# Optimization experiments

Measured on AMD Instinct MI355X. Metric: run time of the kernel, lower is better.

The kernel has to match this reference:

```python
import jax, jax.numpy as jnp
import numpy as np

N = 262144  # nodes
E = 262144  # edges (child -> parent)
X = 128     # x_size
H = 128     # h_size


def setup_inputs() -> dict:
    key = jax.random.key(0)
    ks = jax.random.split(key, 10)
    s = 1.0 / np.sqrt(H)
    return {
        "token_embeds": jax.random.normal(ks[0], (N, X), jnp.float32),
        "h": jax.random.normal(ks[1], (N, H), jnp.float32),
        "c": jax.random.normal(ks[2], (N, H), jnp.float32),
        "src": jax.random.randint(ks[3], (E,), 0, N),
        "dst": jax.random.randint(ks[4], (E,), 0, N),
        "W_iou": jax.random.normal(ks[5], (3 * H, X), jnp.float32) * s,
        "U_iou": jax.random.normal(ks[6], (3 * H, H), jnp.float32) * s,
        "b_iou": jnp.zeros((1, 3 * H), jnp.float32),
        "U_f_w": jax.random.normal(ks[7], (H, H), jnp.float32) * s,
        "U_f_b": jnp.zeros((H,), jnp.float32),
        "W_f_w": jax.random.normal(ks[8], (H, X), jnp.float32) * s,
        "b_f": jnp.zeros((1, H), jnp.float32),
    }


def reference(token_embeds, h, c, src, dst, W_iou, U_iou, b_iou, U_f_w, U_f_b, W_f_w, b_f):
    # message + reduce: gather children's h/c and sum into parent mailboxes
    h_sum = jax.ops.segment_sum(h[src], dst, num_segments=N)  # [N,H]
    c_sum = jax.ops.segment_sum(c[src], dst, num_segments=N)  # [N,H]
    # forget gate is per-node, so sum_k f*c_k == f * sum_k c_k
    f = jax.nn.sigmoid(token_embeds @ W_f_w.T + h @ U_f_w.T + U_f_b + b_f)  # [N,H]
    c_red = f * c_sum
    iou = token_embeds @ W_iou.T + h_sum @ U_iou.T + b_iou  # [N,3H]
    i, o, u = jnp.split(iou, 3, axis=1)
    c_new = jax.nn.sigmoid(i) * jnp.tanh(u) + c_red
    h_new = jax.nn.sigmoid(o) * jnp.tanh(c_new)
    return h_new, c_new
```

## Files before the change

kernel.cpp:

```cpp
#include <hip/hip_runtime.h>
#include <hip/hip_bf16.h>
#include <cstdint>

#define HH 128
#define XX 128

typedef __attribute__((ext_vector_type(8))) short short8;
typedef __attribute__((ext_vector_type(4))) short short4_;
typedef __attribute__((ext_vector_type(4))) float float4_;
typedef __attribute__((ext_vector_type(8))) _Float16 half8_;

__device__ __forceinline__ float sigmoidf_(float x) {
  return 1.f / (1.f + __expf(-x));
}
__device__ __forceinline__ float tanhf_(float x) {
  float e = __expf(-2.f * fabsf(x));
  float t = (1.f - e) / (1.f + e);
  return copysignf(t, x);
}

__global__ __launch_bounds__(256) void hist_kernel(const int* __restrict__ dst,
                                                   int* __restrict__ cnt, int E) {
  int e = blockIdx.x * 256 + threadIdx.x;
  if (e < E) atomicAdd(&cnt[dst[e]], 1);
}

__global__ __launch_bounds__(256) void scan_block_sum(const int* __restrict__ cnt,
                                                      int* __restrict__ bsum) {
  __shared__ int red[256];
  int b = blockIdx.x, t = threadIdx.x;
  int base = b * 1024 + t * 4;
  int s = cnt[base] + cnt[base + 1] + cnt[base + 2] + cnt[base + 3];
  red[t] = s;
  __syncthreads();
  for (int off = 128; off > 0; off >>= 1) {
    if (t < off) red[t] += red[t + off];
    __syncthreads();
  }
  if (t == 0) bsum[b] = red[0];
}

__global__ __launch_bounds__(256) void scan_top(const int* __restrict__ bsum,
                                                int* __restrict__ boff,
                                                int* __restrict__ row_ptr, int N,
                                                int E) {
  __shared__ int tmp[256];
  int t = threadIdx.x;
  int own = bsum[t];
  tmp[t] = own;
  __syncthreads();
  for (int off = 1; off < 256; off <<= 1) {
    int x = (t >= off) ? tmp[t - off] : 0;
    __syncthreads();
    tmp[t] += x;
    __syncthreads();
  }
  boff[t] = tmp[t] - own;
  if (t == 0) row_ptr[N] = E;
}

__global__ __launch_bounds__(256) void scan_fill(const int* __restrict__ cnt,
                                                 const int* __restrict__ boff,
                                                 int* __restrict__ row_ptr,
                                                 int* __restrict__ row_fill) {
  __shared__ int tsum[256];
  int b = blockIdx.x, t = threadIdx.x;
  int base = b * 1024 + t * 4;
  int v0 = cnt[base], v1 = cnt[base + 1], v2 = cnt[base + 2], v3 = cnt[base + 3];
  int s = v0 + v1 + v2 + v3;
  tsum[t] = s;
  __syncthreads();
  for (int off = 1; off < 256; off <<= 1) {
    int x = (t >= off) ? tsum[t - off] : 0;
    __syncthreads();
    tsum[t] += x;
    __syncthreads();
  }
  int excl = tsum[t] - s + boff[b];
  int p0 = excl, p1 = p0 + v0, p2 = p1 + v1, p3 = p2 + v2;
  row_ptr[base] = p0;
  row_ptr[base + 1] = p1;
  row_ptr[base + 2] = p2;
  row_ptr[base + 3] = p3;
  row_fill[base] = p0;
  row_fill[base + 1] = p1;
  row_fill[base + 2] = p2;
  row_fill[base + 3] = p3;
}

__global__ __launch_bounds__(256) void fill_kernel(const int* __restrict__ src,
                                                   const int* __restrict__ dst,
                                                   int* __restrict__ row_fill,
                                                   int* __restrict__ edge_src,
                                                   int E) {
  int e = blockIdx.x * 256 + threadIdx.x;
  if (e >= E) return;
  int pos = atomicAdd(&row_fill[dst[e]], 1);
  edge_src[pos] = src[e];
}

__global__ __launch_bounds__(256) void prep_kernel(
    const float* __restrict__ W_iou, const float* __restrict__ U_iou,
    const float* __restrict__ b_iou, const float* __restrict__ U_f_w,
    const float* __restrict__ U_f_b, const float* __restrict__ W_f_w,
    const float* __restrict__ b_f, unsigned short* __restrict__ Bh,
    float* __restrict__ bias) {
  int tid = blockIdx.x * 256 + threadIdx.x;
  int kg = tid & 3;
  int c16 = (tid >> 2) & 15;
  int ks = (tid >> 6) & 7;
  int w = (tid >> 9) & 7;
  int g = (tid >> 12) & 3;
  int col = w * 16 + c16;
  int kbase = ks * 32 + kg * 8;
#pragma unroll
  for (int j = 0; j < 8; ++j) {
    int k = kbase + j;
    float v;
    if (g < 3) {
      v = (k < 128) ? W_iou[(size_t)(g * 128 + col) * 128 + k]
                    : U_iou[(size_t)(g * 128 + col) * 128 + (k - 128)];
    } else {
      v = (k < 128) ? W_f_w[(size_t)col * 128 + k]
                    : U_f_w[(size_t)col * 128 + (k - 128)];
    }
    Bh[(size_t)tid * 8 + j] = __builtin_bit_cast(unsigned short, (_Float16)v);
  }
  if (tid < 512) {
    int gg = tid >> 7, cc = tid & 127;
    bias[tid] = (gg < 3) ? b_iou[gg * 128 + cc] : (U_f_b[cc] + b_f[cc]);
  }
}


__device__ __forceinline__ void stage_f16(unsigned short* su, int a, int node,
                                          int k4, float4_ v) {
  unsigned short hq[4];
#pragma unroll
  for (int j = 0; j < 4; ++j)
    hq[j] = __builtin_bit_cast(unsigned short, (_Float16)v[j]);
  int off = k4 ^ ((node & 7) << 3);
  *reinterpret_cast<short4_*>(&su[a * 8192 + node * 128 + off]) =
      *reinterpret_cast<const short4_*>(hq);
}

__device__ __forceinline__ half8_ read_frag(const unsigned short* su, int a,
                                            int node, int kbase, int lane) {
  int k = kbase + ((lane >> 4) << 3);
  int off = k ^ ((node & 7) << 3);
  short8 s = *reinterpret_cast<const short8*>(&su[a * 8192 + node * 128 + off]);
  return __builtin_bit_cast(half8_, s);
}

__device__ __forceinline__ int cw(int row, int col) {
  return row * 128 + (col ^ ((row & 7) << 2));
}

__global__ __launch_bounds__(512, 4) void fused_mfma_kernel(
    const float* __restrict__ te, const float* __restrict__ h,
    const float* __restrict__ c, const int* __restrict__ row_ptr,
    const int* __restrict__ edge_src, const unsigned short* __restrict__ Bh,
    const float* __restrict__ bias, float* __restrict__ out_h,
    float* __restrict__ out_c) {
  __shared__ float4_ smem4[5120];
  unsigned short* su = (unsigned short*)smem4;
  float* cf = (float*)smem4 + 12288;

  const int t = threadIdx.x;
  const int node0 = blockIdx.x * 64;

  const int nl = t >> 3;
  const int sub = t & 7;
  const int e0 = row_ptr[node0 + nl];
  const int e1 = row_ptr[node0 + nl + 1];
  int s0 = (e0 < e1) ? edge_src[e0] : 0;
  float4_ ph[4], pc[4];
  if (e0 < e1) {
    const float* hp = h + (size_t)s0 * HH + sub * 16;
    const float* cp = c + (size_t)s0 * HH + sub * 16;
#pragma unroll
    for (int i = 0; i < 4; ++i) {
      ph[i] = *reinterpret_cast<const float4_*>(hp + i * 4);
      pc[i] = *reinterpret_cast<const float4_*>(cp + i * 4);
    }
  }

#pragma unroll
  for (int i = 0; i < 4; ++i) {
    int q = t + i * 512;
    int node = q >> 5;
    int k4 = (q & 31) * 4;
    float4_ v =
        *reinterpret_cast<const float4_*>(te + (size_t)(node0 + node) * XX + k4);
    stage_f16(su, 0, node, k4, v);
    v = *reinterpret_cast<const float4_*>(h + (size_t)(node0 + node) * HH + k4);
    stage_f16(su, 2, node, k4, v);
  }

  {
    float hs[16], cs[16];
#pragma unroll
    for (int j = 0; j < 16; ++j) {
      hs[j] = 0.f;
      cs[j] = 0.f;
    }
    if (e0 < e1) {
#pragma unroll
      for (int i = 0; i < 4; ++i)
#pragma unroll
        for (int j = 0; j < 4; ++j) {
          hs[i * 4 + j] += ph[i][j];
          cs[i * 4 + j] += pc[i][j];
        }
    }
    for (int e = e0 + 1; e < e1; ++e) {
      int s = edge_src[e];
      const float* hp = h + (size_t)s * HH + sub * 16;
      const float* cp = c + (size_t)s * HH + sub * 16;
#pragma unroll
      for (int i = 0; i < 4; ++i) {
        float4_ hv = *reinterpret_cast<const float4_*>(hp + i * 4);
        float4_ cv = *reinterpret_cast<const float4_*>(cp + i * 4);
#pragma unroll
        for (int j = 0; j < 4; ++j) {
          hs[i * 4 + j] += hv[j];
          cs[i * 4 + j] += cv[j];
        }
      }
    }
#pragma unroll
    for (int i = 0; i < 4; ++i) {
      float4_ v = {hs[i * 4], hs[i * 4 + 1], hs[i * 4 + 2], hs[i * 4 + 3]};
      stage_f16(su, 1, nl, sub * 16 + i * 4, v);
      *reinterpret_cast<float4_*>(&cf[cw(nl, sub * 16 + i * 4)]) =
          (float4_){cs[i * 4], cs[i * 4 + 1], cs[i * 4 + 2], cs[i * 4 + 3]};
    }
  }
  __syncthreads();

  const int lane = t & 63;
  const int wave = t >> 6;
  const int wc = wave * 16;
  const int cl = lane & 15;
  const int kq = lane >> 4;

  float4_ acc[4][4];
#pragma unroll
  for (int g = 0; g < 4; ++g) {
    float b = bias[g * 128 + wc + cl];
#pragma unroll
    for (int m = 0; m < 4; ++m) acc[g][m] = (float4_){b, b, b, b};
  }

  for (int ks = 0; ks < 8; ++ks) {
    half8_ bh[4];
#pragma unroll
    for (int g = 0; g < 4; ++g) {
      size_t boff = (size_t)(((g * 8 + wave) * 8 + ks) * 512) + cl * 32 + kq * 8;
      bh[g] = __builtin_bit_cast(half8_,
                                 *reinterpret_cast<const short8*>(&Bh[boff]));
    }
    if (ks < 4) {
      int kbase = ks * 32;
#pragma unroll
      for (int m = 0; m < 4; ++m) {
        half8_ ah = read_frag(su, 0, m * 16 + cl, kbase, lane);
#pragma unroll
        for (int g = 0; g < 4; ++g)
          acc[g][m] =
              __builtin_amdgcn_mfma_f32_16x16x32_f16(ah, bh[g], acc[g][m], 0, 0, 0);
      }
    } else {
      int kbase = (ks - 4) * 32;
#pragma unroll
      for (int m = 0; m < 4; ++m) {
        half8_ ah = read_frag(su, 1, m * 16 + cl, kbase, lane);
        half8_ fh = read_frag(su, 2, m * 16 + cl, kbase, lane);
#pragma unroll
        for (int g = 0; g < 3; ++g)
          acc[g][m] =
              __builtin_amdgcn_mfma_f32_16x16x32_f16(ah, bh[g], acc[g][m], 0, 0, 0);
        acc[3][m] =
            __builtin_amdgcn_mfma_f32_16x16x32_f16(fh, bh[3], acc[3][m], 0, 0, 0);
      }
    }
  }

  float csv[4][4];
#pragma unroll
  for (int m = 0; m < 4; ++m)
#pragma unroll
    for (int r = 0; r < 4; ++r)
      csv[m][r] = cf[cw(m * 16 + kq * 4 + r, wc + cl)];

  __syncthreads();

  float* oh = (float*)smem4;
  float* oc = (float*)smem4 + 8192;

#pragma unroll
  for (int m = 0; m < 4; ++m) {
#pragma unroll
    for (int r = 0; r < 4; ++r) {
      int rowl = m * 16 + kq * 4 + r;
      float ig = sigmoidf_(acc[0][m][r]);
      float og = sigmoidf_(acc[1][m][r]);
      float ug = tanhf_(acc[2][m][r]);
      float fg = sigmoidf_(acc[3][m][r]);
      float cn = fmaf(ig, ug, fg * csv[m][r]);
      int wadr = cw(rowl, wc + cl);
      oc[wadr] = cn;
      oh[wadr] = og * tanhf_(cn);
    }
  }
  __syncthreads();

#pragma unroll
  for (int i = 0; i < 4; ++i) {
    int q = t + i * 512;
    int rr = q >> 5;
    int k4 = (q & 31) * 4;
    int wadr = rr * 128 + (k4 ^ ((rr & 7) << 2));
    *reinterpret_cast<float4_*>(out_h + (size_t)(node0 + rr) * HH + k4) =
        *reinterpret_cast<const float4_*>(&oh[wadr]);
    *reinterpret_cast<float4_*>(out_c + (size_t)(node0 + rr) * HH + k4) =
        *reinterpret_cast<const float4_*>(&oc[wadr]);
  }
}

extern "C" void kernel_launch(void* const* d_in, const int* in_sizes, int n_in,
                              void* d_out, int out_size, void* d_ws, size_t ws_size,
                              hipStream_t stream) {
  const float* te = (const float*)d_in[0];
  const float* h = (const float*)d_in[1];
  const float* c = (const float*)d_in[2];
  const int* src = (const int*)d_in[3];
  const int* dst = (const int*)d_in[4];
  const float* W_iou = (const float*)d_in[5];
  const float* U_iou = (const float*)d_in[6];
  const float* b_iou = (const float*)d_in[7];
  const float* U_f_w = (const float*)d_in[8];
  const float* U_f_b = (const float*)d_in[9];
  const float* W_f_w = (const float*)d_in[10];
  const float* b_f = (const float*)d_in[11];

  const int N = in_sizes[1] / HH;
  const int E = in_sizes[3];

  float* out_h = (float*)d_out;
  float* out_c = out_h + (size_t)N * HH;

  char* ws = (char*)d_ws;
  unsigned short* Bh = (unsigned short*)ws;
  float* bias = (float*)(Bh + 4 * 8 * 8 * 16 * 4 * 8);
  int* cnt = (int*)(bias + 512);
  int* row_ptr = cnt + N;
  int* row_fill = row_ptr + N + 4;
  int* edge_src = row_fill + N;
  int* bsum = edge_src + E;
  int* boff = bsum + 256;

  hipMemsetAsync(cnt, 0, (size_t)N * sizeof(int), stream);

  hist_kernel<<<(E + 255) / 256, 256, 0, stream>>>(dst, cnt, E);
  scan_block_sum<<<N / 1024, 256, 0, stream>>>(cnt, bsum);
  scan_top<<<1, 256, 0, stream>>>(bsum, boff, row_ptr, N, E);
  scan_fill<<<N / 1024, 256, 0, stream>>>(cnt, boff, row_ptr, row_fill);
  fill_kernel<<<(E + 255) / 256, 256, 0, stream>>>(src, dst, row_fill, edge_src, E);

  prep_kernel<<<64, 256, 0, stream>>>(W_iou, U_iou, b_iou, U_f_w, U_f_b, W_f_w,
                                      b_f, Bh, bias);

  fused_mfma_kernel<<<N / 64, 512, 0, stream>>>(te, h, c, row_ptr, edge_src, Bh,
                                                bias, out_h, out_c);
}
```

Baseline: 289.5 us.

## Halve node tile per block and stage child c-sum in fp16 LDS

```diff
diff --git a/kernel.cpp b/kernel.cpp
--- a/kernel.cpp
+++ b/kernel.cpp
@@ -140,7 +140,7 @@
   for (int j = 0; j < 4; ++j)
     hq[j] = __builtin_bit_cast(unsigned short, (_Float16)v[j]);
   int off = k4 ^ ((node & 7) << 3);
-  *reinterpret_cast<short4_*>(&su[a * 8192 + node * 128 + off]) =
+  *reinterpret_cast<short4_*>(&su[a * 4096 + node * 128 + off]) =
       *reinterpret_cast<const short4_*>(hq);
 }
 
@@ -148,7 +148,7 @@
                                             int node, int kbase, int lane) {
   int k = kbase + ((lane >> 4) << 3);
   int off = k ^ ((node & 7) << 3);
-  short8 s = *reinterpret_cast<const short8*>(&su[a * 8192 + node * 128 + off]);
+  short8 s = *reinterpret_cast<const short8*>(&su[a * 4096 + node * 128 + off]);
   return __builtin_bit_cast(half8_, s);
 }
 
@@ -156,18 +156,17 @@
   return row * 128 + (col ^ ((row & 7) << 2));
 }
 
-__global__ __launch_bounds__(512, 4) void fused_mfma_kernel(
+__global__ __launch_bounds__(256, 5) void fused_mfma_kernel(
     const float* __restrict__ te, const float* __restrict__ h,
     const float* __restrict__ c, const int* __restrict__ row_ptr,
     const int* __restrict__ edge_src, const unsigned short* __restrict__ Bh,
     const float* __restrict__ bias, float* __restrict__ out_h,
     float* __restrict__ out_c) {
-  __shared__ float4_ smem4[5120];
+  __shared__ float4_ smem4[2048];
   unsigned short* su = (unsigned short*)smem4;
-  float* cf = (float*)smem4 + 12288;
 
   const int t = threadIdx.x;
-  const int node0 = blockIdx.x * 64;
+  const int node0 = blockIdx.x * 32;
 
   const int nl = t >> 3;
   const int sub = t & 7;
@@ -187,7 +186,7 @@
 
 #pragma unroll
   for (int i = 0; i < 4; ++i) {
-    int q = t + i * 512;
+    int q = t + i * 256;
     int node = q >> 5;
     int k4 = (q & 31) * 4;
     float4_ v =
@@ -232,92 +231,110 @@
     for (int i = 0; i < 4; ++i) {
       float4_ v = {hs[i * 4], hs[i * 4 + 1], hs[i * 4 + 2], hs[i * 4 + 3]};
       stage_f16(su, 1, nl, sub * 16 + i * 4, v);
-      *reinterpret_cast<float4_*>(&cf[cw(nl, sub * 16 + i * 4)]) =
-          (float4_){cs[i * 4], cs[i * 4 + 1], cs[i * 4 + 2], cs[i * 4 + 3]};
+      float4_ cv = {cs[i * 4], cs[i * 4 + 1], cs[i * 4 + 2], cs[i * 4 + 3]};
+      stage_f16(su, 3, nl, sub * 16 + i * 4, cv);
     }
   }
   __syncthreads();
 
   const int lane = t & 63;
   const int wave = t >> 6;
-  const int wc = wave * 16;
+  const int wc = wave * 32;
   const int cl = lane & 15;
   const int kq = lane >> 4;
 
-  float4_ acc[4][4];
-#pragma unroll
-  for (int g = 0; g < 4; ++g) {
-    float b = bias[g * 128 + wc + cl];
-#pragma unroll
-    for (int m = 0; m < 4; ++m) acc[g][m] = (float4_){b, b, b, b};
-  }
+  float4_ acc[4][2][2];
+#pragma unroll
+  for (int g = 0; g < 4; ++g)
+#pragma unroll
+    for (int cg = 0; cg < 2; ++cg) {
+      float b = bias[g * 128 + wc + cg * 16 + cl];
+      acc[g][0][cg] = (float4_){b, b, b, b};
+      acc[g][1][cg] = (float4_){b, b, b, b};
+    }
 
   for (int ks = 0; ks < 8; ++ks) {
-    half8_ bh[4];
-#pragma unroll
-    for (int g = 0; g < 4; ++g) {
-      size_t boff = (size_t)(((g * 8 + wave) * 8 + ks) * 512) + cl * 32 + kq * 8;
-      bh[g] = __builtin_bit_cast(half8_,
-                                 *reinterpret_cast<const short8*>(&Bh[boff]));
-    }
+    half8_ bh[4][2];
+#pragma unroll
+    for (int g = 0; g < 4; ++g)
+#pragma unroll
+      for (int cg = 0; cg < 2; ++cg) {
+        size_t boff =
+            (size_t)(((g * 8 + wave * 2 + cg) * 8 + ks) * 512) + cl * 32 + kq * 8;
+        bh[g][cg] = __builtin_bit_cast(
+            half8_, *reinterpret_cast<const short8*>(&Bh[boff]));
+      }
     if (ks < 4) {
       int kbase = ks * 32;
 #pragma unroll
-      for (int m = 0; m < 4; ++m) {
+      for (int m = 0; m < 2; ++m) {
         half8_ ah = read_frag(su, 0, m * 16 + cl, kbase, lane);
 #pragma unroll
         for (int g = 0; g < 4; ++g)
-          acc[g][m] =
-              __builtin_amdgcn_mfma_f32_16x16x32_f16(ah, bh[g], acc[g][m], 0, 0, 0);
+#pragma unroll
+          for (int cg = 0; cg < 2; ++cg)
+            acc[g][m][cg] = __builtin_amdgcn_mfma_f32_16x16x32_f16(
+                ah, bh[g][cg], acc[g][m][cg], 0, 0, 0);
       }
     } else {
       int kbase = (ks - 4) * 32;
 #pragma unroll
-      for (int m = 0; m < 4; ++m) {
+      for (int m = 0; m < 2; ++m) {
         half8_ ah = read_frag(su, 1, m * 16 + cl, kbase, lane);
         half8_ fh = read_frag(su, 2, m * 16 + cl, kbase, lane);
 #pragma unroll
-        for (int g = 0; g < 3; ++g)
-          acc[g][m] =
-              __builtin_amdgcn_mfma_f32_16x16x32_f16(ah, bh[g], acc[g][m], 0, 0, 0);
-        acc[3][m] =
-            __builtin_amdgcn_mfma_f32_16x16x32_f16(fh, bh[3], acc[3][m], 0, 0, 0);
-      }
-    }
-  }
-
-  float csv[4][4];
-#pragma unroll
-  for (int m = 0; m < 4; ++m)
-#pragma unroll
-    for (int r = 0; r < 4; ++r)
-      csv[m][r] = cf[cw(m * 16 + kq * 4 + r, wc + cl)];
+        for (int cg = 0; cg < 2; ++cg) {
+#pragma unroll
+          for (int g = 0; g < 3; ++g)
+            acc[g][m][cg] = __builtin_amdgcn_mfma_f32_16x16x32_f16(
+                ah, bh[g][cg], acc[g][m][cg], 0, 0, 0);
+          acc[3][m][cg] = __builtin_amdgcn_mfma_f32_16x16x32_f16(
+              fh, bh[3][cg], acc[3][m][cg], 0, 0, 0);
+        }
+      }
+    }
+  }
+
+  float csv[2][2][4];
+#pragma unroll
+  for (int m = 0; m < 2; ++m)
+#pragma unroll
+    for (int cg = 0; cg < 2; ++cg)
+#pragma unroll
+      for (int r = 0; r < 4; ++r) {
+        int row = m * 16 + kq * 4 + r;
+        int col = wc + cg * 16 + cl;
+        unsigned short hb = su[3 * 4096 + row * 128 + (col ^ ((row & 7) << 3))];
+        csv[m][cg][r] = (float)__builtin_bit_cast(_Float16, hb);
+      }
 
   __syncthreads();
 
   float* oh = (float*)smem4;
-  float* oc = (float*)smem4 + 8192;
-
-#pragma unroll
-  for (int m = 0; m < 4; ++m) {
-#pragma unroll
-    for (int r = 0; r < 4; ++r) {
-      int rowl = m * 16 + kq * 4 + r;
-      float ig = sigmoidf_(acc[0][m][r]);
-      float og = sigmoidf_(acc[1][m][r]);
-      float ug = tanhf_(acc[2][m][r]);
-      float fg = sigmoidf_(acc[3][m][r]);
-      float cn = fmaf(ig, ug, fg * csv[m][r]);
-      int wadr = cw(rowl, wc + cl);
-      oc[wadr] = cn;
-      oh[wadr] = og * tanhf_(cn);
-    }
-  }
+  float* oc = (float*)smem4 + 4096;
+
+#pragma unroll
+  for (int m = 0; m < 2; ++m)
+#pragma unroll
+    for (int cg = 0; cg < 2; ++cg)
+#pragma unroll
+      for (int r = 0; r < 4; ++r) {
+        int rowl = m * 16 + kq * 4 + r;
+        int col = wc + cg * 16 + cl;
+        float ig = sigmoidf_(acc[0][m][cg][r]);
+        float og = sigmoidf_(acc[1][m][cg][r]);
+        float ug = tanhf_(acc[2][m][cg][r]);
+        float fg = sigmoidf_(acc[3][m][cg][r]);
+        float cn = fmaf(ig, ug, fg * csv[m][cg][r]);
+        int wadr = cw(rowl, col);
+        oc[wadr] = cn;
+        oh[wadr] = og * tanhf_(cn);
+      }
   __syncthreads();
 
 #pragma unroll
   for (int i = 0; i < 4; ++i) {
-    int q = t + i * 512;
+    int q = t + i * 256;
     int rr = q >> 5;
     int k4 = (q & 31) * 4;
     int wadr = rr * 128 + (k4 ^ ((rr & 7) << 2));
@@ -371,6 +388,6 @@
   prep_kernel<<<64, 256, 0, stream>>>(W_iou, U_iou, b_iou, U_f_w, U_f_b, W_f_w,
                                       b_f, Bh, bias);
 
-  fused_mfma_kernel<<<N / 64, 512, 0, stream>>>(te, h, c, row_ptr, edge_src, Bh,
+  fused_mfma_kernel<<<N / 32, 256, 0, stream>>>(te, h, c, row_ptr, edge_src, Bh,
                                                 bias, out_h, out_c);
 }
```

Result: slower. 673.3 us (+132.5%).

## Halve node tile to 32 and store c-sum as fp16 to raise occupancy

Applied to the files above, without the earlier changes.

```diff
diff --git a/kernel.cpp b/kernel.cpp
--- a/kernel.cpp
+++ b/kernel.cpp
@@ -140,7 +140,7 @@
   for (int j = 0; j < 4; ++j)
     hq[j] = __builtin_bit_cast(unsigned short, (_Float16)v[j]);
   int off = k4 ^ ((node & 7) << 3);
-  *reinterpret_cast<short4_*>(&su[a * 8192 + node * 128 + off]) =
+  *reinterpret_cast<short4_*>(&su[a * 4096 + node * 128 + off]) =
       *reinterpret_cast<const short4_*>(hq);
 }
 
@@ -148,7 +148,7 @@
                                             int node, int kbase, int lane) {
   int k = kbase + ((lane >> 4) << 3);
   int off = k ^ ((node & 7) << 3);
-  short8 s = *reinterpret_cast<const short8*>(&su[a * 8192 + node * 128 + off]);
+  short8 s = *reinterpret_cast<const short8*>(&su[a * 4096 + node * 128 + off]);
   return __builtin_bit_cast(half8_, s);
 }
 
@@ -156,37 +156,36 @@
   return row * 128 + (col ^ ((row & 7) << 2));
 }
 
-__global__ __launch_bounds__(512, 4) void fused_mfma_kernel(
+__global__ __launch_bounds__(512, 6) void fused_mfma_kernel(
     const float* __restrict__ te, const float* __restrict__ h,
     const float* __restrict__ c, const int* __restrict__ row_ptr,
     const int* __restrict__ edge_src, const unsigned short* __restrict__ Bh,
     const float* __restrict__ bias, float* __restrict__ out_h,
     float* __restrict__ out_c) {
-  __shared__ float4_ smem4[5120];
+  __shared__ float4_ smem4[2048];
   unsigned short* su = (unsigned short*)smem4;
-  float* cf = (float*)smem4 + 12288;
 
   const int t = threadIdx.x;
-  const int node0 = blockIdx.x * 64;
-
-  const int nl = t >> 3;
-  const int sub = t & 7;
+  const int node0 = blockIdx.x * 32;
+
+  const int nl = t >> 4;
+  const int sub = t & 15;
   const int e0 = row_ptr[node0 + nl];
   const int e1 = row_ptr[node0 + nl + 1];
   int s0 = (e0 < e1) ? edge_src[e0] : 0;
-  float4_ ph[4], pc[4];
+  float4_ ph[2], pc[2];
   if (e0 < e1) {
-    const float* hp = h + (size_t)s0 * HH + sub * 16;
-    const float* cp = c + (size_t)s0 * HH + sub * 16;
-#pragma unroll
-    for (int i = 0; i < 4; ++i) {
+    const float* hp = h + (size_t)s0 * HH + sub * 8;
+    const float* cp = c + (size_t)s0 * HH + sub * 8;
+#pragma unroll
+    for (int i = 0; i < 2; ++i) {
       ph[i] = *reinterpret_cast<const float4_*>(hp + i * 4);
       pc[i] = *reinterpret_cast<const float4_*>(cp + i * 4);
     }
   }
 
 #pragma unroll
-  for (int i = 0; i < 4; ++i) {
+  for (int i = 0; i < 2; ++i) {
     int q = t + i * 512;
     int node = q >> 5;
     int k4 = (q & 31) * 4;
@@ -198,15 +197,15 @@
   }
 
   {
-    float hs[16], cs[16];
-#pragma unroll
-    for (int j = 0; j < 16; ++j) {
+    float hs[8], cs[8];
+#pragma unroll
+    for (int j = 0; j < 8; ++j) {
       hs[j] = 0.f;
       cs[j] = 0.f;
     }
     if (e0 < e1) {
 #pragma unroll
-      for (int i = 0; i < 4; ++i)
+      for (int i = 0; i < 2; ++i)
 #pragma unroll
         for (int j = 0; j < 4; ++j) {
           hs[i * 4 + j] += ph[i][j];
@@ -215,10 +214,10 @@
     }
     for (int e = e0 + 1; e < e1; ++e) {
       int s = edge_src[e];
-      const float* hp = h + (size_t)s * HH + sub * 16;
-      const float* cp = c + (size_t)s * HH + sub * 16;
-#pragma unroll
-      for (int i = 0; i < 4; ++i) {
+      const float* hp = h + (size_t)s * HH + sub * 8;
+      const float* cp = c + (size_t)s * HH + sub * 8;
+#pragma unroll
+      for (int i = 0; i < 2; ++i) {
         float4_ hv = *reinterpret_cast<const float4_*>(hp + i * 4);
         float4_ cv = *reinterpret_cast<const float4_*>(cp + i * 4);
 #pragma unroll
@@ -229,11 +228,11 @@
       }
     }
 #pragma unroll
-    for (int i = 0; i < 4; ++i) {
+    for (int i = 0; i < 2; ++i) {
       float4_ v = {hs[i * 4], hs[i * 4 + 1], hs[i * 4 + 2], hs[i * 4 + 3]};
-      stage_f16(su, 1, nl, sub * 16 + i * 4, v);
-      *reinterpret_cast<float4_*>(&cf[cw(nl, sub * 16 + i * 4)]) =
-          (float4_){cs[i * 4], cs[i * 4 + 1], cs[i * 4 + 2], cs[i * 4 + 3]};
+      stage_f16(su, 1, nl, sub * 8 + i * 4, v);
+      float4_ cv = {cs[i * 4], cs[i * 4 + 1], cs[i * 4 + 2], cs[i * 4 + 3]};
+      stage_f16(su, 3, nl, sub * 8 + i * 4, cv);
     }
   }
   __syncthreads();
@@ -244,13 +243,11 @@
   const int cl = lane & 15;
   const int kq = lane >> 4;
 
-  float4_ acc[4][4];
-#pragma unroll
-  for (int g = 0; g < 4; ++g) {
-    float b = bias[g * 128 + wc + cl];
-#pragma unroll
-    for (int m = 0; m < 4; ++m) acc[g][m] = (float4_){b, b, b, b};
-  }
+  float4_ acc[4][2];
+#pragma unroll
+  for (int g = 0; g < 4; ++g)
+#pragma unroll
+    for (int m = 0; m < 2; ++m) acc[g][m] = (float4_){0.f, 0.f, 0.f, 0.f};
 
   for (int ks = 0; ks < 8; ++ks) {
     half8_ bh[4];
@@ -263,60 +260,67 @@
     if (ks < 4) {
       int kbase = ks * 32;
 #pragma unroll
-      for (int m = 0; m < 4; ++m) {
+      for (int m = 0; m < 2; ++m) {
         half8_ ah = read_frag(su, 0, m * 16 + cl, kbase, lane);
 #pragma unroll
         for (int g = 0; g < 4; ++g)
-          acc[g][m] =
-              __builtin_amdgcn_mfma_f32_16x16x32_f16(ah, bh[g], acc[g][m], 0, 0, 0);
+          acc[g][m] = __builtin_amdgcn_mfma_f32_16x16x32_f16(ah, bh[g],
+                                                             acc[g][m], 0, 0, 0);
       }
     } else {
       int kbase = (ks - 4) * 32;
 #pragma unroll
-      for (int m = 0; m < 4; ++m) {
+      for (int m = 0; m < 2; ++m) {
         half8_ ah = read_frag(su, 1, m * 16 + cl, kbase, lane);
         half8_ fh = read_frag(su, 2, m * 16 + cl, kbase, lane);
 #pragma unroll
         for (int g = 0; g < 3; ++g)
-          acc[g][m] =
-              __builtin_amdgcn_mfma_f32_16x16x32_f16(ah, bh[g], acc[g][m], 0, 0, 0);
-        acc[3][m] =
-            __builtin_amdgcn_mfma_f32_16x16x32_f16(fh, bh[3], acc[3][m], 0, 0, 0);
+          acc[g][m] = __builtin_amdgcn_mfma_f32_16x16x32_f16(ah, bh[g],
+                                                             acc[g][m], 0, 0, 0);
+        acc[3][m] = __builtin_amdgcn_mfma_f32_16x16x32_f16(fh, bh[3],
+                                                           acc[3][m], 0, 0, 0);
       }
     }
   }
 
-  float csv[4][4];
-#pragma unroll
-  for (int m = 0; m < 4; ++m)
-#pragma unroll
-    for (int r = 0; r < 4; ++r)
-      csv[m][r] = cf[cw(m * 16 + kq * 4 + r, wc + cl)];
+  const int col = wc + cl;
+  float bi = bias[0 * 128 + col];
+  float bo = bias[1 * 128 + col];
+  float bu = bias[2 * 128 + col];
+  float bf = bias[3 * 128 + col];
+  float csv[2][4];
+#pragma unroll
+  for (int m = 0; m < 2; ++m)
+#pragma unroll
+    for (int r = 0; r < 4; ++r) {
+      int row = m * 16 + kq * 4 + r;
+      unsigned short hb = su[3 * 4096 + row * 128 + (col ^ ((row & 7) << 3))];
+      csv[m][r] = (float)__builtin_bit_cast(_Float16, hb);
+    }
 
   __syncthreads();
 
   float* oh = (float*)smem4;
-  float* oc = (float*)smem4 + 8192;
-
-#pragma unroll
-  for (int m = 0; m < 4; ++m) {
+  float* oc = (float*)smem4 + 4096;
+
+#pragma unroll
+  for (int m = 0; m < 2; ++m)
 #pragma unroll
     for (int r = 0; r < 4; ++r) {
       int rowl = m * 16 + kq * 4 + r;
-      float ig = sigmoidf_(acc[0][m][r]);
-      float og = sigmoidf_(acc[1][m][r]);
-      float ug = tanhf_(acc[2][m][r]);
-      float fg = sigmoidf_(acc[3][m][r]);
+      float ig = sigmoidf_(acc[0][m][r] + bi);
+      float og = sigmoidf_(acc[1][m][r] + bo);
+      float ug = tanhf_(acc[2][m][r] + bu);
+      float fg = sigmoidf_(acc[3][m][r] + bf);
       float cn = fmaf(ig, ug, fg * csv[m][r]);
-      int wadr = cw(rowl, wc + cl);
+      int wadr = cw(rowl, col);
       oc[wadr] = cn;
       oh[wadr] = og * tanhf_(cn);
     }
-  }
-  __syncthreads();
-
-#pragma unroll
-  for (int i = 0; i < 4; ++i) {
+  __syncthreads();
+
+#pragma unroll
+  for (int i = 0; i < 2; ++i) {
     int q = t + i * 512;
     int rr = q >> 5;
     int k4 = (q & 31) * 4;
@@ -371,6 +375,6 @@
   prep_kernel<<<64, 256, 0, stream>>>(W_iou, U_iou, b_iou, U_f_w, U_f_b, W_f_w,
                                       b_f, Bh, bias);
 
-  fused_mfma_kernel<<<N / 64, 512, 0, stream>>>(te, h, c, row_ptr, edge_src, Bh,
+  fused_mfma_kernel<<<N / 32, 512, 0, stream>>>(te, h, c, row_ptr, edge_src, Bh,
                                                 bias, out_h, out_c);
 }
```

Result: slower. 321.9 us (+11.2%).

## Load MFMA A-fragments for te and h directly from global, shrink LDS to fp16

Applied to the files above, without the earlier changes.

```diff
diff --git a/kernel.cpp b/kernel.cpp
--- a/kernel.cpp
+++ b/kernel.cpp
@@ -6,9 +6,9 @@
 #define XX 128
 
 typedef __attribute__((ext_vector_type(8))) short short8;
-typedef __attribute__((ext_vector_type(4))) short short4_;
 typedef __attribute__((ext_vector_type(4))) float float4_;
 typedef __attribute__((ext_vector_type(8))) _Float16 half8_;
+typedef __attribute__((ext_vector_type(4))) unsigned int uint4_;
 
 __device__ __forceinline__ float sigmoidf_(float x) {
   return 1.f / (1.f + __expf(-x));
@@ -133,27 +133,30 @@
 }
 
 
-__device__ __forceinline__ void stage_f16(unsigned short* su, int a, int node,
-                                          int k4, float4_ v) {
-  unsigned short hq[4];
-#pragma unroll
-  for (int j = 0; j < 4; ++j)
-    hq[j] = __builtin_bit_cast(unsigned short, (_Float16)v[j]);
-  int off = k4 ^ ((node & 7) << 3);
-  *reinterpret_cast<short4_*>(&su[a * 8192 + node * 128 + off]) =
-      *reinterpret_cast<const short4_*>(hq);
-}
-
-__device__ __forceinline__ half8_ read_frag(const unsigned short* su, int a,
+__device__ __forceinline__ uint4_ pack8(const float* v) {
+  uint4_ r;
+#pragma unroll
+  for (int i = 0; i < 4; ++i)
+    r[i] = __builtin_bit_cast(unsigned int,
+                              __builtin_amdgcn_cvt_pkrtz(v[2 * i], v[2 * i + 1]));
+  return r;
+}
+
+__device__ __forceinline__ half8_ cvt8(float4_ a, float4_ b) {
+  uint4_ u;
+  u[0] = __builtin_bit_cast(unsigned int, __builtin_amdgcn_cvt_pkrtz(a[0], a[1]));
+  u[1] = __builtin_bit_cast(unsigned int, __builtin_amdgcn_cvt_pkrtz(a[2], a[3]));
+  u[2] = __builtin_bit_cast(unsigned int, __builtin_amdgcn_cvt_pkrtz(b[0], b[1]));
+  u[3] = __builtin_bit_cast(unsigned int, __builtin_amdgcn_cvt_pkrtz(b[2], b[3]));
+  return __builtin_bit_cast(half8_, u);
+}
+
+__device__ __forceinline__ half8_ read_frag(const unsigned short* su, int baseH,
                                             int node, int kbase, int lane) {
   int k = kbase + ((lane >> 4) << 3);
   int off = k ^ ((node & 7) << 3);
-  short8 s = *reinterpret_cast<const short8*>(&su[a * 8192 + node * 128 + off]);
+  short8 s = *reinterpret_cast<const short8*>(&su[baseH + node * 128 + off]);
   return __builtin_bit_cast(half8_, s);
-}
-
-__device__ __forceinline__ int cw(int row, int col) {
-  return row * 128 + (col ^ ((row & 7) << 2));
 }
 
 __global__ __launch_bounds__(512, 4) void fused_mfma_kernel(
@@ -162,58 +165,24 @@
     const int* __restrict__ edge_src, const unsigned short* __restrict__ Bh,
     const float* __restrict__ bias, float* __restrict__ out_h,
     float* __restrict__ out_c) {
-  __shared__ float4_ smem4[5120];
+  __shared__ float4_ smem4[2048];
   unsigned short* su = (unsigned short*)smem4;
-  float* cf = (float*)smem4 + 12288;
 
   const int t = threadIdx.x;
   const int node0 = blockIdx.x * 64;
 
-  const int nl = t >> 3;
-  const int sub = t & 7;
-  const int e0 = row_ptr[node0 + nl];
-  const int e1 = row_ptr[node0 + nl + 1];
-  int s0 = (e0 < e1) ? edge_src[e0] : 0;
-  float4_ ph[4], pc[4];
-  if (e0 < e1) {
-    const float* hp = h + (size_t)s0 * HH + sub * 16;
-    const float* cp = c + (size_t)s0 * HH + sub * 16;
-#pragma unroll
-    for (int i = 0; i < 4; ++i) {
-      ph[i] = *reinterpret_cast<const float4_*>(hp + i * 4);
-      pc[i] = *reinterpret_cast<const float4_*>(cp + i * 4);
-    }
-  }
-
-#pragma unroll
-  for (int i = 0; i < 4; ++i) {
-    int q = t + i * 512;
-    int node = q >> 5;
-    int k4 = (q & 31) * 4;
-    float4_ v =
-        *reinterpret_cast<const float4_*>(te + (size_t)(node0 + node) * XX + k4);
-    stage_f16(su, 0, node, k4, v);
-    v = *reinterpret_cast<const float4_*>(h + (size_t)(node0 + node) * HH + k4);
-    stage_f16(su, 2, node, k4, v);
-  }
-
   {
+    const int nl = t >> 3;
+    const int sub = t & 7;
+    const int e0 = row_ptr[node0 + nl];
+    const int e1 = row_ptr[node0 + nl + 1];
     float hs[16], cs[16];
 #pragma unroll
     for (int j = 0; j < 16; ++j) {
       hs[j] = 0.f;
       cs[j] = 0.f;
     }
-    if (e0 < e1) {
-#pragma unroll
-      for (int i = 0; i < 4; ++i)
-#pragma unroll
-        for (int j = 0; j < 4; ++j) {
-          hs[i * 4 + j] += ph[i][j];
-          cs[i * 4 + j] += pc[i][j];
-        }
-    }
-    for (int e = e0 + 1; e < e1; ++e) {
+    for (int e = e0; e < e1; ++e) {
       int s = edge_src[e];
       const float* hp = h + (size_t)s * HH + sub * 16;
       const float* cp = c + (size_t)s * HH + sub * 16;
@@ -229,11 +198,10 @@
       }
     }
 #pragma unroll
-    for (int i = 0; i < 4; ++i) {
-      float4_ v = {hs[i * 4], hs[i * 4 + 1], hs[i * 4 + 2], hs[i * 4 + 3]};
-      stage_f16(su, 1, nl, sub * 16 + i * 4, v);
-      *reinterpret_cast<float4_*>(&cf[cw(nl, sub * 16 + i * 4)]) =
-          (float4_){cs[i * 4], cs[i * 4 + 1], cs[i * 4 + 2], cs[i * 4 + 3]};
+    for (int i = 0; i < 2; ++i) {
+      int off = (sub * 16 + i * 8) ^ ((nl & 7) << 3);
+      *reinterpret_cast<uint4_*>(&su[nl * 128 + off]) = pack8(hs + i * 8);
+      *reinterpret_cast<uint4_*>(&su[8192 + nl * 128 + off]) = pack8(cs + i * 8);
     }
   }
   __syncthreads();
@@ -243,14 +211,16 @@
   const int wc = wave * 16;
   const int cl = lane & 15;
   const int kq = lane >> 4;
+  const int col = wc + cl;
+
+  const float* teF = te + (size_t)(node0 + cl) * XX + kq * 8;
+  const float* hF = h + (size_t)(node0 + cl) * HH + kq * 8;
 
   float4_ acc[4][4];
 #pragma unroll
-  for (int g = 0; g < 4; ++g) {
-    float b = bias[g * 128 + wc + cl];
-#pragma unroll
-    for (int m = 0; m < 4; ++m) acc[g][m] = (float4_){b, b, b, b};
-  }
+  for (int g = 0; g < 4; ++g)
+#pragma unroll
+    for (int m = 0; m < 4; ++m) acc[g][m] = (float4_){0.f, 0.f, 0.f, 0.f};
 
   for (int ks = 0; ks < 8; ++ks) {
     half8_ bh[4];
@@ -264,67 +234,83 @@
       int kbase = ks * 32;
 #pragma unroll
       for (int m = 0; m < 4; ++m) {
-        half8_ ah = read_frag(su, 0, m * 16 + cl, kbase, lane);
+        const float* p = teF + (size_t)m * 16 * XX + kbase;
+        half8_ ah = cvt8(*reinterpret_cast<const float4_*>(p),
+                         *reinterpret_cast<const float4_*>(p + 4));
 #pragma unroll
         for (int g = 0; g < 4; ++g)
-          acc[g][m] =
-              __builtin_amdgcn_mfma_f32_16x16x32_f16(ah, bh[g], acc[g][m], 0, 0, 0);
+          acc[g][m] = __builtin_amdgcn_mfma_f32_16x16x32_f16(ah, bh[g],
+                                                             acc[g][m], 0, 0, 0);
       }
     } else {
       int kbase = (ks - 4) * 32;
 #pragma unroll
       for (int m = 0; m < 4; ++m) {
-        half8_ ah = read_frag(su, 1, m * 16 + cl, kbase, lane);
-        half8_ fh = read_frag(su, 2, m * 16 + cl, kbase, lane);
+        half8_ ah = read_frag(su, 0, m * 16 + cl, kbase, lane);
+        const float* p = hF + (size_t)m * 16 * HH + kbase;
+        half8_ fh = cvt8(*reinterpret_cast<const float4_*>(p),
+                         *reinterpret_cast<const float4_*>(p + 4));
 #pragma unroll
         for (int g = 0; g < 3; ++g)
-          acc[g][m] =
-              __builtin_amdgcn_mfma_f32_16x16x32_f16(ah, bh[g], acc[g][m], 0, 0, 0);
-        acc[3][m] =
-            __builtin_amdgcn_mfma_f32_16x16x32_f16(fh, bh[3], acc[3][m], 0, 0, 0);
+          acc[g][m] = __builtin_amdgcn_mfma_f32_16x16x32_f16(ah, bh[g],
+                                                             acc[g][m], 0, 0, 0);
+        acc[3][m] = __builtin_amdgcn_mfma_f32_16x16x32_f16(fh, bh[3],
+                                                           acc[3][m], 0, 0, 0);
       }
     }
   }
 
+  const float bi = bias[col];
+  const float bo = bias[128 + col];
+  const float bu = bias[256 + col];
+  const float bf = bias[384 + col];
   float csv[4][4];
 #pragma unroll
   for (int m = 0; m < 4; ++m)
 #pragma unroll
-    for (int r = 0; r < 4; ++r)
-      csv[m][r] = cf[cw(m * 16 + kq * 4 + r, wc + cl)];
-
-  __syncthreads();
-
-  float* oh = (float*)smem4;
-  float* oc = (float*)smem4 + 8192;
-
-#pragma unroll
-  for (int m = 0; m < 4; ++m) {
-#pragma unroll
     for (int r = 0; r < 4; ++r) {
-      int rowl = m * 16 + kq * 4 + r;
-      float ig = sigmoidf_(acc[0][m][r]);
-      float og = sigmoidf_(acc[1][m][r]);
-      float ug = tanhf_(acc[2][m][r]);
-      float fg = sigmoidf_(acc[3][m][r]);
+      int row = m * 16 + kq * 4 + r;
+      unsigned short hb = su[8192 + row * 128 + (col ^ ((row & 7) << 3))];
+      csv[m][r] = (float)__builtin_bit_cast(_Float16, hb);
+    }
+  __syncthreads();
+
+#pragma unroll
+  for (int m = 0; m < 4; ++m)
+#pragma unroll
+    for (int r = 0; r < 4; ++r) {
+      int row = m * 16 + kq * 4 + r;
+      float ig = sigmoidf_(acc[0][m][r] + bi);
+      float og = sigmoidf_(acc[1][m][r] + bo);
+      float ug = tanhf_(acc[2][m][r] + bu);
+      float fg = sigmoidf_(acc[3][m][r] + bf);
       float cn = fmaf(ig, ug, fg * csv[m][r]);
-      int wadr = cw(rowl, wc + cl);
-      oc[wadr] = cn;
-      oh[wadr] = og * tanhf_(cn);
-    }
-  }
+      float hn = og * tanhf_(cn);
+      int off = col ^ ((row & 7) << 3);
+      su[row * 128 + off] = __builtin_bit_cast(unsigned short, (_Float16)hn);
+      su[8192 + row * 128 + off] = __builtin_bit_cast(unsigned short, (_Float16)cn);
+    }
   __syncthreads();
 
 #pragma unroll
   for (int i = 0; i < 4; ++i) {
     int q = t + i * 512;
-    int rr = q >> 5;
-    int k4 = (q & 31) * 4;
-    int wadr = rr * 128 + (k4 ^ ((rr & 7) << 2));
-    *reinterpret_cast<float4_*>(out_h + (size_t)(node0 + rr) * HH + k4) =
-        *reinterpret_cast<const float4_*>(&oh[wadr]);
-    *reinterpret_cast<float4_*>(out_c + (size_t)(node0 + rr) * HH + k4) =
-        *reinterpret_cast<const float4_*>(&oc[wadr]);
+    int arr = q >> 10;
+    int cq = q & 1023;
+    int rr = cq >> 4;
+    int k8 = (cq & 15) * 8;
+    short8 v = *reinterpret_cast<const short8*>(
+        &su[arr * 8192 + rr * 128 + (k8 ^ ((rr & 7) << 3))]);
+    half8_ hv = __builtin_bit_cast(half8_, v);
+    float4_ f0, f1;
+#pragma unroll
+    for (int j = 0; j < 4; ++j) {
+      f0[j] = (float)hv[j];
+      f1[j] = (float)hv[4 + j];
+    }
+    float* outp = (arr ? out_c : out_h) + (size_t)(node0 + rr) * HH + k8;
+    *reinterpret_cast<float4_*>(outp) = f0;
+    *reinterpret_cast<float4_*>(outp + 4) = f1;
   }
 }
 
```

New measurement: 454.5 us. +57.0%, slower.
